# Optimization experiments

Hardware: AMD Instinct MI355X
Metric: run time of the kernel (lower is better)

## Reference

```python
import jax, jax.numpy as jnp
import numpy as np

G = 2            # num codevector groups
C = 320          # codes per group
VQ_DIM = 256     # codevector_dim
D = VQ_DIM // G  # per-group code dim = 128
TAU = 2.0        # gumbel temperature


def setup_inputs() -> dict:
    key = jax.random.key(0)
    k1, k2, k3, k4, k5, k6 = jax.random.split(key, 6)
    B, T, H = 16, 3072, 512
    x = jax.random.normal(k1, (B, T, H), dtype=jnp.float32)
    masked_token_idx = jax.random.randint(k2, (B, T), 0, 2) > 0  # bool mask
    gumbel_noise = jax.random.gumbel(k3, (B * T * G, C), dtype=jnp.float32)
    q_proj_w = jax.random.normal(k4, (G * C, H), dtype=jnp.float32) * (1.0 / np.sqrt(H))
    q_proj_b = jax.random.normal(k5, (G * C,), dtype=jnp.float32) * 0.02
    codevectors = jax.random.uniform(k6, (1, G * C, D), dtype=jnp.float32)
    return {"x": x, "masked_token_idx": masked_token_idx, "gumbel_noise": gumbel_noise,
            "q_proj_w": q_proj_w, "q_proj_b": q_proj_b, "codevectors": codevectors}


def _perplexity(probs, mask_flat):
    # probs: [B*T, G, C]; masked mean over tokens, then per-codebook perplexity
    m = mask_flat.astype(probs.dtype)
    denom = jnp.maximum(m.sum(), 1.0)
    p = jnp.einsum('ngc,n->gc', probs, m) / denom  # [G, C]
    perp_per_cb = jnp.exp(-jnp.sum(p * jnp.log(p + 1e-7), axis=-1))
    return perp_per_cb.sum()


def reference(x, masked_token_idx, gumbel_noise, q_proj_w, q_proj_b, codevectors):
    B, T, H = x.shape
    N = B * T
    logits = jnp.einsum('bth,kh->btk', x, q_proj_w) + q_proj_b  # [B,T,G*C]
    l = logits.reshape(N * G, C)
    # hard gumbel-softmax with straight-through estimator (training path)
    y_soft = jax.nn.softmax((l + gumbel_noise) / TAU, axis=-1)
    idx = jnp.argmax(y_soft, axis=-1)
    y_hard = jax.nn.one_hot(idx, C, dtype=y_soft.dtype)
    codevector_probs = y_hard + y_soft - jax.lax.stop_gradient(y_soft)  # [N*G, C]
    # perplexity from plain (non-tempered) softmax of logits, over masked tokens
    soft = jax.nn.softmax(l.reshape(N, G, C), axis=-1)
    perplexity = _perplexity(soft, masked_token_idx.reshape(-1))
    # codevector gather-multiply-sum, expressed as a grouped contraction
    # (same math as probs.unsqueeze(-1)*codevectors then sum over codes)
    cv = codevectors.reshape(G, C, D)
    probs3 = codevector_probs.reshape(N, G, C)
    selected = jnp.einsum('ngc,gcd->ngd', probs3, cv).reshape(B, T, G * D)
    return selected, perplexity
```

## Files before the change

### kernel.cpp

```cpp
#include <hip/hip_runtime.h>
#include <hip/hip_bf16.h>
#include <math.h>

#define TOKS 49152
#define HD   512
#define GN   2
#define CN   320
#define DN   128
#define BM   64
#define NTHR 512
#define LSTR 324

#define BH_OFF 0
#define BL_OFF 20480
#define AH_OFF 40960
#define AL_OFF 45056
#define SBUF   49152
#define SMEM_DYN (2 * SBUF)
#define PSUM_OFF 41472

#define BMF  32
#define NTHRF 256
#define WSTR 33

#define WS_WELEMS ((size_t)(GN * CN) * HD)
#define WS_W_OFF  4096
#define WS_MID    (WS_W_OFF + 4 * WS_WELEMS)

typedef _Float16 f16x8 __attribute__((ext_vector_type(8)));
typedef float    fx4   __attribute__((ext_vector_type(4)));

#define GLD_LDS16(gp, lp)                                                    \
  __builtin_amdgcn_global_load_lds(                                          \
      (const __attribute__((address_space(1))) void*)(gp),                   \
      (__attribute__((address_space(3))) void*)(lp), 16, 0, 0)

__global__ void k_zero(float* pp) {
  int t = threadIdx.x;
  if (t < GN * CN) pp[t] = 0.f;
}

__global__ __launch_bounds__(256) void k_split(const float* __restrict__ src,
                                               _Float16* __restrict__ dh,
                                               _Float16* __restrict__ dl,
                                               float* __restrict__ pp) {
  if (blockIdx.x < 3) {
    int i = blockIdx.x * 256 + threadIdx.x;
    if (i < GN * CN) pp[i] = 0.f;
  }
  size_t t    = (size_t)blockIdx.x * 256 + threadIdx.x;
  int    lane = (int)(t & 63);
  size_t blob = t >> 6;
  int    k0   = (int)(blob & 15);
  size_t rb   = blob >> 4;
  const float* p = src + (rb * 16 + (lane & 15)) * HD + k0 * 32 + (lane >> 4) * 8;
  fx4 u = *(const fx4*)p;
  fx4 v = *(const fx4*)(p + 4);
  f16x8 h8, l8;
  #pragma unroll
  for (int e = 0; e < 4; ++e) {
    _Float16 hu = (_Float16)u[e], hv = (_Float16)v[e];
    h8[e]     = hu;
    h8[e + 4] = hv;
    l8[e]     = (_Float16)((u[e] - (float)hu) * 512.f);
    l8[e + 4] = (_Float16)((v[e] - (float)hv) * 512.f);
  }
  *(f16x8*)(dh + t * 8) = h8;
  *(f16x8*)(dl + t * 8) = l8;
}

__global__ __launch_bounds__(NTHR, 2) void k_gemm_ep(
    const float* __restrict__ x, const int* __restrict__ mask,
    const float* __restrict__ gnoise, const float* __restrict__ bias,
    const float* __restrict__ cv, const _Float16* __restrict__ wh,
    const _Float16* __restrict__ wl, float* __restrict__ out,
    float* __restrict__ pp)
{
  extern __shared__ __align__(16) char smem[];
  float* lg   = (float*)smem;
  float* psum = (float*)(smem + PSUM_OFF);

  const int u   = blockIdx.x;
  const int mt  = ((u >> 4) << 3) | (u & 7);
  const int g   = (u >> 3) & 1;
  const int m0  = mt * BM;
  const int tid = threadIdx.x;
  const int tc  = tid & 63;
  const int w   = tid >> 6;
  const int wr  = w >> 2;
  const int wc  = w & 3;
  const int l15 = tid & 15;
  const int l4  = tc >> 4;

  fx4 aH[2][5], aL[2][5];
  #pragma unroll
  for (int rf = 0; rf < 2; ++rf)
    #pragma unroll
    for (int cf = 0; cf < 5; ++cf) {
      aH[rf][cf] = (fx4){0.f, 0.f, 0.f, 0.f};
      aL[rf][cf] = (fx4){0.f, 0.f, 0.f, 0.f};
    }

  const _Float16* bb = (w < 4) ? wh : wl;
  const int cb0      = (w < 4) ? w * 5 : w * 5 - 20;
  const _Float16* bsrc = bb + (size_t)(g * 20 + cb0) * 8192 + (size_t)tc * 8;
  const int arow = tid >> 2;
  const int al4  = tid & 3;
  const float* asrc = x + (size_t)(m0 + arow) * HD + al4 * 8;
  const int aslot = (arow >> 4) * 1024 + ((arow & 15) + 16 * al4) * 16;

#define STAGE(T, BASE) do {                                                  \
    _Pragma("unroll")                                                        \
    for (int q = 0; q < 5; ++q)                                              \
      GLD_LDS16(bsrc + (size_t)q * 8192 + (size_t)(T) * 512,                 \
                (BASE) + w * 5120 + q * 1024);                               \
    if (tid < 256) {                                                         \
      fx4 au = *(const fx4*)(asrc + (size_t)(T) * 32);                       \
      fx4 av = *(const fx4*)(asrc + (size_t)(T) * 32 + 4);                   \
      f16x8 h8, l8;                                                          \
      _Pragma("unroll")                                                      \
      for (int e = 0; e < 4; ++e) {                                          \
        _Float16 hh;                                                         \
        hh = (_Float16)au[e]; h8[e] = hh;                                    \
        l8[e] = (_Float16)((au[e] - (float)hh) * 512.f);                     \
        hh = (_Float16)av[e]; h8[e + 4] = hh;                                \
        l8[e + 4] = (_Float16)((av[e] - (float)hh) * 512.f);                 \
      }                                                                      \
      *(f16x8*)((BASE) + AH_OFF + aslot) = h8;                               \
      *(f16x8*)((BASE) + AL_OFF + aslot) = l8;                               \
    }                                                                        \
  } while (0)

#define COMPUTE(BASE) do {                                                   \
    f16x8 A0h = *(const f16x8*)((BASE) + AH_OFF + (wr * 2 + 0) * 1024 + tc * 16); \
    f16x8 A1h = *(const f16x8*)((BASE) + AH_OFF + (wr * 2 + 1) * 1024 + tc * 16); \
    f16x8 A0l = *(const f16x8*)((BASE) + AL_OFF + (wr * 2 + 0) * 1024 + tc * 16); \
    f16x8 A1l = *(const f16x8*)((BASE) + AL_OFF + (wr * 2 + 1) * 1024 + tc * 16); \
    _Pragma("unroll")                                                        \
    for (int cf = 0; cf < 5; ++cf) {                                         \
      f16x8 Bh = *(const f16x8*)((BASE) + BH_OFF + (wc * 5 + cf) * 1024 + tc * 16); \
      f16x8 Bl = *(const f16x8*)((BASE) + BL_OFF + (wc * 5 + cf) * 1024 + tc * 16); \
      aH[0][cf] = __builtin_amdgcn_mfma_f32_16x16x32_f16(A0h, Bh, aH[0][cf], 0, 0, 0); \
      aH[1][cf] = __builtin_amdgcn_mfma_f32_16x16x32_f16(A1h, Bh, aH[1][cf], 0, 0, 0); \
      aL[0][cf] = __builtin_amdgcn_mfma_f32_16x16x32_f16(A0h, Bl, aL[0][cf], 0, 0, 0); \
      aL[0][cf] = __builtin_amdgcn_mfma_f32_16x16x32_f16(A0l, Bh, aL[0][cf], 0, 0, 0); \
      aL[1][cf] = __builtin_amdgcn_mfma_f32_16x16x32_f16(A1h, Bl, aL[1][cf], 0, 0, 0); \
      aL[1][cf] = __builtin_amdgcn_mfma_f32_16x16x32_f16(A1l, Bh, aL[1][cf], 0, 0, 0); \
    }                                                                        \
  } while (0)

  STAGE(0, smem);
  __syncthreads();
  #pragma unroll 2
  for (int t = 0; t < 16; ++t) {
    char* cur = smem + (size_t)(t & 1) * SBUF;
    char* nxt = smem + (size_t)((t & 1) ^ 1) * SBUF;
    if (t < 15) STAGE(t + 1, nxt);
    COMPUTE(cur);
    __syncthreads();
  }
#undef STAGE
#undef COMPUTE

  float bj[5];
  #pragma unroll
  for (int cf = 0; cf < 5; ++cf) bj[cf] = bias[g * CN + wc * 80 + cf * 16 + l15];

  float pacc[5] = {0.f, 0.f, 0.f, 0.f, 0.f};
  #pragma unroll
  for (int p = 0; p < 2; ++p) {
    if (wr == p) {
      #pragma unroll
      for (int cf = 0; cf < 5; ++cf) {
        const int col = wc * 80 + cf * 16 + l15;
        #pragma unroll
        for (int rf = 0; rf < 2; ++rf)
          #pragma unroll
          for (int e = 0; e < 4; ++e)
            lg[(rf * 16 + l4 * 4 + e) * LSTR + col] =
                aH[rf][cf][e] + aL[rf][cf][e] * (1.f / 512.f) + bj[cf];
      }
    }
    __syncthreads();
    #pragma unroll
    for (int i = 0; i < 4; ++i) {
      const int rl = w * 4 + i;
      const int n  = m0 + p * 32 + rl;
      const size_t grow = ((size_t)n * GN + g) * CN;
      float lv[5], gv[5];
      #pragma unroll
      for (int j = 0; j < 5; ++j) lv[j] = lg[rl * LSTR + tc + 64 * j];
      #pragma unroll
      for (int j = 0; j < 5; ++j) gv[j] = gnoise[grow + tc + 64 * j];

      float bv = -3.4e38f; int bi = 1 << 30;
      #pragma unroll
      for (int j = 0; j < 5; ++j) {
        float v = lv[j] + gv[j];
        if (v > bv) { bv = v; bi = tc + 64 * j; }
      }
      for (int off = 1; off < 64; off <<= 1) {
        float ov = __shfl_xor(bv, off);
        int   oi = __shfl_xor(bi, off);
        if (ov > bv || (ov == bv && oi < bi)) { bv = ov; bi = oi; }
      }

      float mx = lv[0];
      #pragma unroll
      for (int j = 1; j < 5; ++j) mx = fmaxf(mx, lv[j]);
      for (int off = 1; off < 64; off <<= 1) mx = fmaxf(mx, __shfl_xor(mx, off));
      float e[5], s = 0.f;
      #pragma unroll
      for (int j = 0; j < 5; ++j) { e[j] = __expf(lv[j] - mx); s += e[j]; }
      for (int off = 1; off < 64; off <<= 1) s += __shfl_xor(s, off);
      const float inv = 1.f / s;
      const float mlt = (mask[n] != 0) ? 1.f : 0.f;
      #pragma unroll
      for (int j = 0; j < 5; ++j) pacc[j] += mlt * e[j] * inv;

      const float2* cvr = (const float2*)(cv + ((size_t)(g * CN + bi)) * DN);
      float2* o2 = (float2*)(out + (size_t)n * (GN * DN) + g * DN);
      o2[tc] = cvr[tc];
    }
    __syncthreads();
  }

  #pragma unroll
  for (int j = 0; j < 5; ++j) psum[w * CN + tc + 64 * j] = pacc[j];
  __syncthreads();
  for (int c = tid; c < CN; c += NTHR) {
    float s = 0.f;
    #pragma unroll
    for (int q = 0; q < 8; ++q) s += psum[q * CN + c];
    atomicAdd(&pp[g * CN + c], s);
  }
}

__global__ __launch_bounds__(NTHRF) void k_main_fp32(
    const float* __restrict__ x, const int* __restrict__ mask,
    const float* __restrict__ gnoise, const float* __restrict__ W,
    const float* __restrict__ bias, const float* __restrict__ cv,
    float* __restrict__ out, float* __restrict__ pp)
{
  __shared__ __align__(16) char fsmem[47360];
  float* w_lds = (float*)fsmem;
  float* xs    = (float*)(fsmem + 42240);
  float* lgf   = (float*)fsmem;
  float* psum  = (float*)(fsmem + 42240);

  const int m0  = blockIdx.x * BMF;
  const int g   = blockIdx.y;
  const int tid = threadIdx.x;
  const int tc  = tid & 63;
  const int tr  = tid >> 6;
  const int r0  = tr * 8;

  float acc[8][5];
  #pragma unroll
  for (int i = 0; i < 8; ++i)
    #pragma unroll
    for (int j = 0; j < 5; ++j) acc[i][j] = 0.f;

  const float* Wg = W + (size_t)g * CN * HD;

  for (int k0 = 0; k0 < HD; k0 += 32) {
    __syncthreads();
    #pragma unroll
    for (int t = 0; t < 10; ++t) {
      int idx = tid + t * NTHRF;
      int c   = idx >> 3;
      int k4  = idx & 7;
      float4 wv4 = *(const float4*)(Wg + (size_t)c * HD + k0 + k4 * 4);
      float* dst = &w_lds[c * WSTR + k4 * 4];
      dst[0] = wv4.x; dst[1] = wv4.y; dst[2] = wv4.z; dst[3] = wv4.w;
    }
    {
      int r = tid >> 3, k4 = tid & 7;
      float4 xv = *(const float4*)(x + (size_t)(m0 + r) * HD + k0 + k4 * 4);
      float* dst = &xs[r * 32 + k4 * 4];
      dst[0] = xv.x; dst[1] = xv.y; dst[2] = xv.z; dst[3] = xv.w;
    }
    __syncthreads();
    #pragma unroll
    for (int kk = 0; kk < 32; kk += 4) {
      float xq[8][4];
      #pragma unroll
      for (int i = 0; i < 8; ++i) {
        float4 t4 = *(const float4*)&xs[(r0 + i) * 32 + kk];
        xq[i][0] = t4.x; xq[i][1] = t4.y; xq[i][2] = t4.z; xq[i][3] = t4.w;
      }
      #pragma unroll
      for (int q = 0; q < 4; ++q) {
        float wv[5];
        #pragma unroll
        for (int j = 0; j < 5; ++j) wv[j] = w_lds[(tc + 64 * j) * WSTR + kk + q];
        #pragma unroll
        for (int i = 0; i < 8; ++i)
          #pragma unroll
          for (int j = 0; j < 5; ++j)
            acc[i][j] = fmaf(xq[i][q], wv[j], acc[i][j]);
      }
    }
  }
  __syncthreads();

  float bj[5];
  #pragma unroll
  for (int j = 0; j < 5; ++j) bj[j] = bias[g * CN + tc + 64 * j];
  #pragma unroll
  for (int i = 0; i < 8; ++i)
    #pragma unroll
    for (int j = 0; j < 5; ++j)
      lgf[(r0 + i) * CN + tc + 64 * j] = acc[i][j] + bj[j];
  __syncthreads();

  float pacc[5] = {0.f, 0.f, 0.f, 0.f, 0.f};
  #pragma unroll
  for (int i = 0; i < 8; ++i) {
    const int r = r0 + i;
    const int n = m0 + r;
    const size_t grow = ((size_t)n * GN + g) * CN;
    float lv[5], gv[5];
    #pragma unroll
    for (int j = 0; j < 5; ++j) lv[j] = lgf[r * CN + tc + 64 * j];
    #pragma unroll
    for (int j = 0; j < 5; ++j) gv[j] = gnoise[grow + tc + 64 * j];

    float bv = -3.4e38f; int bi = 1 << 30;
    #pragma unroll
    for (int j = 0; j < 5; ++j) {
      float v = lv[j] + gv[j];
      if (v > bv) { bv = v; bi = tc + 64 * j; }
    }
    for (int off = 1; off < 64; off <<= 1) {
      float ov = __shfl_xor(bv, off);
      int   oi = __shfl_xor(bi, off);
      if (ov > bv || (ov == bv && oi < bi)) { bv = ov; bi = oi; }
    }

    float mx = lv[0];
    #pragma unroll
    for (int j = 1; j < 5; ++j) mx = fmaxf(mx, lv[j]);
    for (int off = 1; off < 64; off <<= 1) mx = fmaxf(mx, __shfl_xor(mx, off));
    float e[5], s = 0.f;
    #pragma unroll
    for (int j = 0; j < 5; ++j) { e[j] = expf(lv[j] - mx); s += e[j]; }
    for (int off = 1; off < 64; off <<= 1) s += __shfl_xor(s, off);
    const float inv = 1.f / s;
    const float mlt = (mask[n] != 0) ? 1.f : 0.f;
    #pragma unroll
    for (int j = 0; j < 5; ++j) pacc[j] += mlt * e[j] * inv;

    const float2* cvr = (const float2*)(cv + ((size_t)(g * CN + bi)) * DN);
    float2* o2 = (float2*)(out + (size_t)n * (GN * DN) + g * DN);
    o2[tc] = cvr[tc];
  }

  #pragma unroll
  for (int j = 0; j < 5; ++j) psum[tr * CN + tc + 64 * j] = pacc[j];
  __syncthreads();
  for (int c = tid; c < CN; c += NTHRF) {
    float s = psum[c] + psum[CN + c] + psum[2 * CN + c] + psum[3 * CN + c];
    atomicAdd(&pp[g * CN + c], s);
  }
}

__global__ __launch_bounds__(640) void k_final(
    const float* __restrict__ pp, const int* __restrict__ mask,
    float* __restrict__ out, int out_off)
{
  __shared__ float red[10];
  __shared__ float eL[GN * CN];
  __shared__ float perp_parts[GN];
  const int tid = threadIdx.x;

  float cnt = 0.f;
  for (int i = tid; i < TOKS; i += 640) cnt += (mask[i] != 0) ? 1.f : 0.f;
  for (int off = 1; off < 64; off <<= 1) cnt += __shfl_xor(cnt, off);
  if ((tid & 63) == 0) red[tid >> 6] = cnt;
  __syncthreads();
  float denom = 0.f;
  #pragma unroll
  for (int w = 0; w < 10; ++w) denom += red[w];
  denom = fmaxf(denom, 1.f);

  const float p = pp[tid] / denom;
  eL[tid] = p * logf(p + 1e-7f);
  __syncthreads();

  if (tid < 2 * 64) {
    const int gg = tid >> 6, ll = tid & 63;
    float s = 0.f;
    #pragma unroll
    for (int j = 0; j < 5; ++j) s += eL[gg * CN + ll + 64 * j];
    for (int off = 1; off < 64; off <<= 1) s += __shfl_xor(s, off);
    if (ll == 0) perp_parts[gg] = expf(-s);
  }
  __syncthreads();
  if (tid == 0) out[out_off] = perp_parts[0] + perp_parts[1];
}

extern "C" void kernel_launch(void* const* d_in, const int* in_sizes, int n_in,
                              void* d_out, int out_size, void* d_ws, size_t ws_size,
                              hipStream_t stream) {
  const float* x     = (const float*)d_in[0];
  const int*   mask  = (const int*)d_in[1];
  const float* gn    = (const float*)d_in[2];
  const float* W     = (const float*)d_in[3];
  const float* bias  = (const float*)d_in[4];
  const float* cv    = (const float*)d_in[5];
  float* out = (float*)d_out;
  float* pp  = (float*)d_ws;

  if (ws_size >= WS_MID) {
    _Float16* wh = (_Float16*)((char*)d_ws + WS_W_OFF);
    _Float16* wl = wh + WS_WELEMS;
    hipLaunchKernelGGL(k_split, dim3((int)(WS_WELEMS / 8 / 256)), dim3(256), 0,
                       stream, W, wh, wl, pp);
    hipLaunchKernelGGL(k_gemm_ep, dim3(TOKS / BM * GN), dim3(NTHR), SMEM_DYN,
                       stream, x, mask, gn, bias, cv, wh, wl, out, pp);
  } else {
    hipLaunchKernelGGL(k_zero, dim3(1), dim3(640), 0, stream, pp);
    hipLaunchKernelGGL(k_main_fp32, dim3(TOKS / BMF, GN), dim3(NTHRF), 0, stream,
                       x, mask, gn, W, bias, cv, out, pp);
  }

  hipLaunchKernelGGL(k_final, dim3(1), dim3(640), 0, stream,
                     pp, mask, out, out_size - 1);
}
```

Before: 231.2 us.

## Double GEMM row tile to 128 and split A staging around compute

Raises the per-block token tile from 64 to 128 rows, so each staged weight tile feeds twice as many MFMAs and B-tile reuse rises. All 512 threads now load the fp32 activations, with the load issued before compute and the fp16 hi/lo split plus LDS write done after compute, so global latency is hidden behind the MFMAs. This costs more accumulator registers (40 fx4) and more LDS, which may lower occupancy, and halves the block count. The block-index mapping (mt derived from u) is not visibly changed, so the grid size must also shrink elsewhere for coverage to stay correct.

```diff
diff --git a/kernel.cpp b/kernel.cpp
--- a/kernel.cpp
+++ b/kernel.cpp
@@ -7,17 +7,17 @@
 #define GN   2
 #define CN   320
 #define DN   128
-#define BM   64
+#define BM   128
 #define NTHR 512
 #define LSTR 324
 
 #define BH_OFF 0
 #define BL_OFF 20480
 #define AH_OFF 40960
-#define AL_OFF 45056
-#define SBUF   49152
+#define AL_OFF 49152
+#define SBUF   57344
 #define SMEM_DYN (2 * SBUF)
-#define PSUM_OFF 41472
+#define PSUM_OFF 82944
 
 #define BMF  32
 #define NTHRF 256
@@ -92,9 +92,9 @@
   const int l15 = tid & 15;
   const int l4  = tc >> 4;
 
-  fx4 aH[2][5], aL[2][5];
-  #pragma unroll
-  for (int rf = 0; rf < 2; ++rf)
+  fx4 aH[4][5], aL[4][5];
+  #pragma unroll
+  for (int rf = 0; rf < 4; ++rf)
     #pragma unroll
     for (int cf = 0; cf < 5; ++cf) {
       aH[rf][cf] = (fx4){0.f, 0.f, 0.f, 0.f};
@@ -104,62 +104,81 @@
   const _Float16* bb = (w < 4) ? wh : wl;
   const int cb0      = (w < 4) ? w * 5 : w * 5 - 20;
   const _Float16* bsrc = bb + (size_t)(g * 20 + cb0) * 8192 + (size_t)tc * 8;
-  const int arow = tid >> 2;
-  const int al4  = tid & 3;
-  const float* asrc = x + (size_t)(m0 + arow) * HD + al4 * 8;
-  const int aslot = (arow >> 4) * 1024 + ((arow & 15) + 16 * al4) * 16;
-
-#define STAGE(T, BASE) do {                                                  \
+  const float* asrc = x + (size_t)(m0 + w * 16 + (tc & 15)) * HD + (tc >> 4) * 8;
+  const int aslot = w * 1024 + tc * 16;
+
+  fx4 au, av;
+
+#define STAGE_A_LOAD(T) do {                                                 \
+    au = *(const fx4*)(asrc + (size_t)(T) * 32);                             \
+    av = *(const fx4*)(asrc + (size_t)(T) * 32 + 4);                         \
+  } while (0)
+
+#define STAGE_B(T, BASE) do {                                                \
     _Pragma("unroll")                                                        \
     for (int q = 0; q < 5; ++q)                                              \
       GLD_LDS16(bsrc + (size_t)q * 8192 + (size_t)(T) * 512,                 \
                 (BASE) + w * 5120 + q * 1024);                               \
-    if (tid < 256) {                                                         \
-      fx4 au = *(const fx4*)(asrc + (size_t)(T) * 32);                       \
-      fx4 av = *(const fx4*)(asrc + (size_t)(T) * 32 + 4);                   \
-      f16x8 h8, l8;                                                          \
-      _Pragma("unroll")                                                      \
-      for (int e = 0; e < 4; ++e) {                                          \
-        _Float16 hh;                                                         \
-        hh = (_Float16)au[e]; h8[e] = hh;                                    \
-        l8[e] = (_Float16)((au[e] - (float)hh) * 512.f);                     \
-        hh = (_Float16)av[e]; h8[e + 4] = hh;                                \
-        l8[e + 4] = (_Float16)((av[e] - (float)hh) * 512.f);                 \
-      }                                                                      \
-      *(f16x8*)((BASE) + AH_OFF + aslot) = h8;                               \
-      *(f16x8*)((BASE) + AL_OFF + aslot) = l8;                               \
+  } while (0)
+
+#define STAGE_A_WRITE(BASE) do {                                             \
+    f16x8 h8, l8;                                                            \
+    _Pragma("unroll")                                                        \
+    for (int e = 0; e < 4; ++e) {                                            \
+      _Float16 hh;                                                           \
+      hh = (_Float16)au[e]; h8[e] = hh;                                      \
+      l8[e] = (_Float16)((au[e] - (float)hh) * 512.f);                       \
+      hh = (_Float16)av[e]; h8[e + 4] = hh;                                  \
+      l8[e + 4] = (_Float16)((av[e] - (float)hh) * 512.f);                   \
     }                                                                        \
+    *(f16x8*)((BASE) + AH_OFF + aslot) = h8;                                 \
+    *(f16x8*)((BASE) + AL_OFF + aslot) = l8;                                 \
   } while (0)
 
 #define COMPUTE(BASE) do {                                                   \
-    f16x8 A0h = *(const f16x8*)((BASE) + AH_OFF + (wr * 2 + 0) * 1024 + tc * 16); \
-    f16x8 A1h = *(const f16x8*)((BASE) + AH_OFF + (wr * 2 + 1) * 1024 + tc * 16); \
-    f16x8 A0l = *(const f16x8*)((BASE) + AL_OFF + (wr * 2 + 0) * 1024 + tc * 16); \
-    f16x8 A1l = *(const f16x8*)((BASE) + AL_OFF + (wr * 2 + 1) * 1024 + tc * 16); \
+    f16x8 Ah0 = *(const f16x8*)((BASE) + AH_OFF + (wr * 4 + 0) * 1024 + tc * 16); \
+    f16x8 Ah1 = *(const f16x8*)((BASE) + AH_OFF + (wr * 4 + 1) * 1024 + tc * 16); \
+    f16x8 Ah2 = *(const f16x8*)((BASE) + AH_OFF + (wr * 4 + 2) * 1024 + tc * 16); \
+    f16x8 Ah3 = *(const f16x8*)((BASE) + AH_OFF + (wr * 4 + 3) * 1024 + tc * 16); \
+    f16x8 Al0 = *(const f16x8*)((BASE) + AL_OFF + (wr * 4 + 0) * 1024 + tc * 16); \
+    f16x8 Al1 = *(const f16x8*)((BASE) + AL_OFF + (wr * 4 + 1) * 1024 + tc * 16); \
+    f16x8 Al2 = *(const f16x8*)((BASE) + AL_OFF + (wr * 4 + 2) * 1024 + tc * 16); \
+    f16x8 Al3 = *(const f16x8*)((BASE) + AL_OFF + (wr * 4 + 3) * 1024 + tc * 16); \
     _Pragma("unroll")                                                        \
     for (int cf = 0; cf < 5; ++cf) {                                         \
       f16x8 Bh = *(const f16x8*)((BASE) + BH_OFF + (wc * 5 + cf) * 1024 + tc * 16); \
       f16x8 Bl = *(const f16x8*)((BASE) + BL_OFF + (wc * 5 + cf) * 1024 + tc * 16); \
-      aH[0][cf] = __builtin_amdgcn_mfma_f32_16x16x32_f16(A0h, Bh, aH[0][cf], 0, 0, 0); \
-      aH[1][cf] = __builtin_amdgcn_mfma_f32_16x16x32_f16(A1h, Bh, aH[1][cf], 0, 0, 0); \
-      aL[0][cf] = __builtin_amdgcn_mfma_f32_16x16x32_f16(A0h, Bl, aL[0][cf], 0, 0, 0); \
-      aL[0][cf] = __builtin_amdgcn_mfma_f32_16x16x32_f16(A0l, Bh, aL[0][cf], 0, 0, 0); \
-      aL[1][cf] = __builtin_amdgcn_mfma_f32_16x16x32_f16(A1h, Bl, aL[1][cf], 0, 0, 0); \
-      aL[1][cf] = __builtin_amdgcn_mfma_f32_16x16x32_f16(A1l, Bh, aL[1][cf], 0, 0, 0); \
+      aH[0][cf] = __builtin_amdgcn_mfma_f32_16x16x32_f16(Ah0, Bh, aH[0][cf], 0, 0, 0); \
+      aH[1][cf] = __builtin_amdgcn_mfma_f32_16x16x32_f16(Ah1, Bh, aH[1][cf], 0, 0, 0); \
+      aH[2][cf] = __builtin_amdgcn_mfma_f32_16x16x32_f16(Ah2, Bh, aH[2][cf], 0, 0, 0); \
+      aH[3][cf] = __builtin_amdgcn_mfma_f32_16x16x32_f16(Ah3, Bh, aH[3][cf], 0, 0, 0); \
+      aL[0][cf] = __builtin_amdgcn_mfma_f32_16x16x32_f16(Ah0, Bl, aL[0][cf], 0, 0, 0); \
+      aL[0][cf] = __builtin_amdgcn_mfma_f32_16x16x32_f16(Al0, Bh, aL[0][cf], 0, 0, 0); \
+      aL[1][cf] = __builtin_amdgcn_mfma_f32_16x16x32_f16(Ah1, Bl, aL[1][cf], 0, 0, 0); \
+      aL[1][cf] = __builtin_amdgcn_mfma_f32_16x16x32_f16(Al1, Bh, aL[1][cf], 0, 0, 0); \
+      aL[2][cf] = __builtin_amdgcn_mfma_f32_16x16x32_f16(Ah2, Bl, aL[2][cf], 0, 0, 0); \
+      aL[2][cf] = __builtin_amdgcn_mfma_f32_16x16x32_f16(Al2, Bh, aL[2][cf], 0, 0, 0); \
+      aL[3][cf] = __builtin_amdgcn_mfma_f32_16x16x32_f16(Ah3, Bl, aL[3][cf], 0, 0, 0); \
+      aL[3][cf] = __builtin_amdgcn_mfma_f32_16x16x32_f16(Al3, Bh, aL[3][cf], 0, 0, 0); \
     }                                                                        \
   } while (0)
 
-  STAGE(0, smem);
+  STAGE_A_LOAD(0);
+  STAGE_B(0, smem);
+  STAGE_A_WRITE(smem);
   __syncthreads();
   #pragma unroll 2
   for (int t = 0; t < 16; ++t) {
     char* cur = smem + (size_t)(t & 1) * SBUF;
     char* nxt = smem + (size_t)((t & 1) ^ 1) * SBUF;
-    if (t < 15) STAGE(t + 1, nxt);
+    if (t < 15) { STAGE_A_LOAD(t + 1); STAGE_B(t + 1, nxt); }
     COMPUTE(cur);
+    if (t < 15) STAGE_A_WRITE(nxt);
     __syncthreads();
   }
-#undef STAGE
+#undef STAGE_A_LOAD
+#undef STAGE_B
+#undef STAGE_A_WRITE
 #undef COMPUTE
 
   float bj[5];
@@ -174,7 +193,7 @@
       for (int cf = 0; cf < 5; ++cf) {
         const int col = wc * 80 + cf * 16 + l15;
         #pragma unroll
-        for (int rf = 0; rf < 2; ++rf)
+        for (int rf = 0; rf < 4; ++rf)
           #pragma unroll
           for (int e = 0; e < 4; ++e)
             lg[(rf * 16 + l4 * 4 + e) * LSTR + col] =
@@ -183,9 +202,9 @@
     }
     __syncthreads();
     #pragma unroll
-    for (int i = 0; i < 4; ++i) {
-      const int rl = w * 4 + i;
-      const int n  = m0 + p * 32 + rl;
+    for (int i = 0; i < 8; ++i) {
+      const int rl = w * 8 + i;
+      const int n  = m0 + p * 64 + rl;
       const size_t grow = ((size_t)n * GN + g) * CN;
       float lv[5], gv[5];
       #pragma unroll
```

Measured after the change: 207.9 us, median of 2. 10.1% less time.

## Double M tile, load A fragments directly to registers, split hi/lo MFMA phases

Applied to the files above, without the earlier changes.

Raises the row tile from 64 to 128 rows per block so each wave holds four row fragments. The A operand is no longer split and staged through LDS: it is loaded from global memory into registers and converted to fp16 hi/lo pairs there. The K loop is split into a high-weight phase and a low-weight phase, using explicit vmcnt waits, raw barriers and s_setprio so that B loads overlap the MFMAs. This halves how many times the weights are re-read and cuts LDS traffic, at the cost of many more accumulator registers and lower occupancy.

```diff
diff --git a/kernel.cpp b/kernel.cpp
--- a/kernel.cpp
+++ b/kernel.cpp
@@ -7,19 +7,15 @@
 #define GN   2
 #define CN   320
 #define DN   128
-#define BM   64
+#define BM   128
 #define NTHR 512
 #define LSTR 324
 
-#define BH_OFF 0
-#define BL_OFF 20480
-#define AH_OFF 40960
-#define AL_OFF 45056
-#define SBUF   49152
-#define SMEM_DYN (2 * SBUF)
+#define SBUF   40960
+#define SMEM_DYN 81920
 #define PSUM_OFF 41472
 
-#define BMF  32
+#define BMF 32
 #define NTHRF 256
 #define WSTR 33
 
@@ -34,6 +30,13 @@
   __builtin_amdgcn_global_load_lds(                                          \
       (const __attribute__((address_space(1))) void*)(gp),                   \
       (__attribute__((address_space(3))) void*)(lp), 16, 0, 0)
+
+#define MFMA16(A, B, C) __builtin_amdgcn_mfma_f32_16x16x32_f16(A, B, C, 0, 0, 0)
+
+#define BAR() do { asm volatile("" ::: "memory");                            \
+    __builtin_amdgcn_s_barrier();                                            \
+    asm volatile("" ::: "memory"); } while (0)
+#define WAITVM(N) asm volatile("s_waitcnt vmcnt(" #N ")" ::: "memory")
 
 __global__ void k_zero(float* pp) {
   int t = threadIdx.x;
@@ -92,75 +95,131 @@
   const int l15 = tid & 15;
   const int l4  = tc >> 4;
 
-  fx4 aH[2][5], aL[2][5];
-  #pragma unroll
-  for (int rf = 0; rf < 2; ++rf)
+  fx4 aH[4][5], aL[4][5];
+  #pragma unroll
+  for (int rf = 0; rf < 4; ++rf)
     #pragma unroll
     for (int cf = 0; cf < 5; ++cf) {
       aH[rf][cf] = (fx4){0.f, 0.f, 0.f, 0.f};
       aL[rf][cf] = (fx4){0.f, 0.f, 0.f, 0.f};
     }
 
-  const _Float16* bb = (w < 4) ? wh : wl;
-  const int cb0      = (w < 4) ? w * 5 : w * 5 - 20;
-  const _Float16* bsrc = bb + (size_t)(g * 20 + cb0) * 8192 + (size_t)tc * 8;
-  const int arow = tid >> 2;
-  const int al4  = tid & 3;
-  const float* asrc = x + (size_t)(m0 + arow) * HD + al4 * 8;
-  const int aslot = (arow >> 4) * 1024 + ((arow & 15) + 16 * al4) * 16;
-
-#define STAGE(T, BASE) do {                                                  \
+  const _Float16* whg = wh + (size_t)(g * 20) * 8192 + (size_t)tc * 8;
+  const _Float16* wlg = wl + (size_t)(g * 20) * 8192 + (size_t)tc * 8;
+  const float* ax = x + (size_t)(m0 + wr * 64 + l15) * HD + l4 * 8;
+
+  fx4 u0, v0, u1, v1, u2, v2, u3, v3;
+  f16x8 Ah0, Ah1, Ah2, Ah3, Al0, Al1, Al2, Al3;
+
+#define STAGE_BH(T, BASE) do {                                               \
+    GLD_LDS16(whg + (size_t)(2*w)   * 8192 + (size_t)(T) * 512,              \
+              (BASE) + (2*w)   * 1024);                                      \
+    GLD_LDS16(whg + (size_t)(2*w+1) * 8192 + (size_t)(T) * 512,              \
+              (BASE) + (2*w+1) * 1024);                                      \
+    if (w < 4)                                                               \
+      GLD_LDS16(whg + (size_t)(16+w) * 8192 + (size_t)(T) * 512,             \
+                (BASE) + (16+w) * 1024);                                     \
+  } while (0)
+
+#define STAGE_BL(T, BASE) do {                                               \
+    GLD_LDS16(wlg + (size_t)(2*w)   * 8192 + (size_t)(T) * 512,              \
+              (BASE) + 20480 + (2*w)   * 1024);                              \
+    GLD_LDS16(wlg + (size_t)(2*w+1) * 8192 + (size_t)(T) * 512,              \
+              (BASE) + 20480 + (2*w+1) * 1024);                              \
+    if (w >= 4)                                                              \
+      GLD_LDS16(wlg + (size_t)(12+w) * 8192 + (size_t)(T) * 512,             \
+                (BASE) + 20480 + (12+w) * 1024);                             \
+  } while (0)
+
+#define ISSUE_A(T) do {                                                      \
+    const float* _p = ax + (T) * 32;                                         \
+    u0 = *(const fx4*)(_p);             v0 = *(const fx4*)(_p + 4);          \
+    u1 = *(const fx4*)(_p + 16*HD);     v1 = *(const fx4*)(_p + 16*HD + 4);  \
+    u2 = *(const fx4*)(_p + 32*HD);     v2 = *(const fx4*)(_p + 32*HD + 4);  \
+    u3 = *(const fx4*)(_p + 48*HD);     v3 = *(const fx4*)(_p + 48*HD + 4);  \
+  } while (0)
+
+#define CVT1(U, V, HH, LL) do {                                              \
     _Pragma("unroll")                                                        \
-    for (int q = 0; q < 5; ++q)                                              \
-      GLD_LDS16(bsrc + (size_t)q * 8192 + (size_t)(T) * 512,                 \
-                (BASE) + w * 5120 + q * 1024);                               \
-    if (tid < 256) {                                                         \
-      fx4 au = *(const fx4*)(asrc + (size_t)(T) * 32);                       \
-      fx4 av = *(const fx4*)(asrc + (size_t)(T) * 32 + 4);                   \
-      f16x8 h8, l8;                                                          \
-      _Pragma("unroll")                                                      \
-      for (int e = 0; e < 4; ++e) {                                          \
-        _Float16 hh;                                                         \
-        hh = (_Float16)au[e]; h8[e] = hh;                                    \
-        l8[e] = (_Float16)((au[e] - (float)hh) * 512.f);                     \
-        hh = (_Float16)av[e]; h8[e + 4] = hh;                                \
-        l8[e + 4] = (_Float16)((av[e] - (float)hh) * 512.f);                 \
-      }                                                                      \
-      *(f16x8*)((BASE) + AH_OFF + aslot) = h8;                               \
-      *(f16x8*)((BASE) + AL_OFF + aslot) = l8;                               \
-    }                                                                        \
-  } while (0)
-
-#define COMPUTE(BASE) do {                                                   \
-    f16x8 A0h = *(const f16x8*)((BASE) + AH_OFF + (wr * 2 + 0) * 1024 + tc * 16); \
-    f16x8 A1h = *(const f16x8*)((BASE) + AH_OFF + (wr * 2 + 1) * 1024 + tc * 16); \
-    f16x8 A0l = *(const f16x8*)((BASE) + AL_OFF + (wr * 2 + 0) * 1024 + tc * 16); \
-    f16x8 A1l = *(const f16x8*)((BASE) + AL_OFF + (wr * 2 + 1) * 1024 + tc * 16); \
+    for (int e = 0; e < 4; ++e) {                                            \
+      _Float16 hh;                                                           \
+      hh = (_Float16)U[e]; HH[e] = hh;                                       \
+      LL[e]   = (_Float16)((U[e] - (float)hh) * 512.f);                      \
+      hh = (_Float16)V[e]; HH[e+4] = hh;                                     \
+      LL[e+4] = (_Float16)((V[e] - (float)hh) * 512.f);                      \
+    } } while (0)
+
+#define CVT_A() do { CVT1(u0,v0,Ah0,Al0); CVT1(u1,v1,Ah1,Al1);               \
+                     CVT1(u2,v2,Ah2,Al2); CVT1(u3,v3,Ah3,Al3); } while (0)
+
+#define MFMA_HI(CUR)                                                         \
     _Pragma("unroll")                                                        \
     for (int cf = 0; cf < 5; ++cf) {                                         \
-      f16x8 Bh = *(const f16x8*)((BASE) + BH_OFF + (wc * 5 + cf) * 1024 + tc * 16); \
-      f16x8 Bl = *(const f16x8*)((BASE) + BL_OFF + (wc * 5 + cf) * 1024 + tc * 16); \
-      aH[0][cf] = __builtin_amdgcn_mfma_f32_16x16x32_f16(A0h, Bh, aH[0][cf], 0, 0, 0); \
-      aH[1][cf] = __builtin_amdgcn_mfma_f32_16x16x32_f16(A1h, Bh, aH[1][cf], 0, 0, 0); \
-      aL[0][cf] = __builtin_amdgcn_mfma_f32_16x16x32_f16(A0h, Bl, aL[0][cf], 0, 0, 0); \
-      aL[0][cf] = __builtin_amdgcn_mfma_f32_16x16x32_f16(A0l, Bh, aL[0][cf], 0, 0, 0); \
-      aL[1][cf] = __builtin_amdgcn_mfma_f32_16x16x32_f16(A1h, Bl, aL[1][cf], 0, 0, 0); \
-      aL[1][cf] = __builtin_amdgcn_mfma_f32_16x16x32_f16(A1l, Bh, aL[1][cf], 0, 0, 0); \
-    }                                                                        \
-  } while (0)
-
-  STAGE(0, smem);
-  __syncthreads();
-  #pragma unroll 2
-  for (int t = 0; t < 16; ++t) {
+      f16x8 Bh = *(const f16x8*)((CUR) + (wc*5+cf)*1024 + tc*16);            \
+      aH[0][cf] = MFMA16(Ah0, Bh, aH[0][cf]);                                \
+      aH[1][cf] = MFMA16(Ah1, Bh, aH[1][cf]);                                \
+      aH[2][cf] = MFMA16(Ah2, Bh, aH[2][cf]);                                \
+      aH[3][cf] = MFMA16(Ah3, Bh, aH[3][cf]);                                \
+      aL[0][cf] = MFMA16(Al0, Bh, aL[0][cf]);                                \
+      aL[1][cf] = MFMA16(Al1, Bh, aL[1][cf]);                                \
+      aL[2][cf] = MFMA16(Al2, Bh, aL[2][cf]);                                \
+      aL[3][cf] = MFMA16(Al3, Bh, aL[3][cf]);                                \
+    }
+
+#define MFMA_LO(CUR)                                                         \
+    _Pragma("unroll")                                                        \
+    for (int cf = 0; cf < 5; ++cf) {                                         \
+      f16x8 Bl = *(const f16x8*)((CUR) + 20480 + (wc*5+cf)*1024 + tc*16);    \
+      aL[0][cf] = MFMA16(Ah0, Bl, aL[0][cf]);                                \
+      aL[1][cf] = MFMA16(Ah1, Bl, aL[1][cf]);                                \
+      aL[2][cf] = MFMA16(Ah2, Bl, aL[2][cf]);                                \
+      aL[3][cf] = MFMA16(Ah3, Bl, aL[3][cf]);                                \
+    }
+
+  STAGE_BH(0, smem);
+  ISSUE_A(0);
+  STAGE_BL(0, smem);
+  CVT_A();
+
+  #pragma unroll 1
+  for (int t = 0; t < 15; ++t) {
     char* cur = smem + (size_t)(t & 1) * SBUF;
     char* nxt = smem + (size_t)((t & 1) ^ 1) * SBUF;
-    if (t < 15) STAGE(t + 1, nxt);
-    COMPUTE(cur);
-    __syncthreads();
-  }
-#undef STAGE
-#undef COMPUTE
+    STAGE_BH(t + 1, nxt);
+    WAITVM(13);
+    BAR();
+    __builtin_amdgcn_s_setprio(1);
+    MFMA_HI(cur);
+    __builtin_amdgcn_s_setprio(0);
+    BAR();
+    ISSUE_A(t + 1);
+    STAGE_BL(t + 1, nxt);
+    WAITVM(13);
+    BAR();
+    __builtin_amdgcn_s_setprio(1);
+    MFMA_LO(cur);
+    __builtin_amdgcn_s_setprio(0);
+    CVT_A();
+    BAR();
+  }
+  {
+    char* cur = smem + SBUF;
+    WAITVM(10);
+    BAR();
+    MFMA_HI(cur);
+    BAR();
+    WAITVM(0);
+    BAR();
+    MFMA_LO(cur);
+    BAR();
+  }
+#undef STAGE_BH
+#undef STAGE_BL
+#undef ISSUE_A
+#undef CVT1
+#undef CVT_A
+#undef MFMA_HI
+#undef MFMA_LO
 
   float bj[5];
   #pragma unroll
@@ -168,17 +227,19 @@
 
   float pacc[5] = {0.f, 0.f, 0.f, 0.f, 0.f};
   #pragma unroll
-  for (int p = 0; p < 2; ++p) {
-    if (wr == p) {
-      #pragma unroll
-      for (int cf = 0; cf < 5; ++cf) {
-        const int col = wc * 80 + cf * 16 + l15;
+  for (int p = 0; p < 4; ++p) {
+    if (wr == (p >> 1)) {
+      #pragma unroll
+      for (int q = 0; q < 2; ++q) {
+        const int rf = (p & 1) * 2 + q;
         #pragma unroll
-        for (int rf = 0; rf < 2; ++rf)
+        for (int cf = 0; cf < 5; ++cf) {
+          const int col = wc * 80 + cf * 16 + l15;
           #pragma unroll
           for (int e = 0; e < 4; ++e)
-            lg[(rf * 16 + l4 * 4 + e) * LSTR + col] =
+            lg[(q * 16 + l4 * 4 + e) * LSTR + col] =
                 aH[rf][cf][e] + aL[rf][cf][e] * (1.f / 512.f) + bj[cf];
+        }
       }
     }
     __syncthreads();
```

Measured after the change: 284.8 us. +23.2%, slower.
